# Kernel tuning notes

Hardware: AMD Instinct MI355X
Metric: run time of the kernel (lower is better)

## Reference

```python
import jax, jax.numpy as jnp
import numpy as np

EPSILON = 1e-8
MAX_WEIGHT = 0.15
N_ITER = 20
STEP_SIZE = 0.05
B, P = 32768, 45


def _simplex_projection(w):
    # clamp + renormalize, done twice (differentiable approximation)
    w = jnp.clip(w, 0.0, MAX_WEIGHT)
    w = w / (jnp.sum(w, axis=-1, keepdims=True) + EPSILON)
    w = jnp.clip(w, 0.0, MAX_WEIGHT)
    w = w / (jnp.sum(w, axis=-1, keepdims=True) + EPSILON)
    return w


def setup_inputs() -> dict:
    key = jax.random.key(0)
    k1, k2 = jax.random.split(key, 2)
    # SPD-ish covariance for a well-behaved iterative solve
    A = jax.random.normal(k1, (B, P, P), dtype=jnp.float32) * 0.1
    sigma = jnp.einsum('bij,bkj->bik', A, A) + 0.1 * jnp.eye(P, dtype=jnp.float32)
    beta = jax.nn.softmax(jax.random.normal(k2, (B, P), dtype=jnp.float32), axis=-1)
    w_prev = jnp.full((B, P), 1.0 / P, dtype=jnp.float32)
    return {
        'sigma': sigma,
        'beta': beta,
        'w_prev': w_prev,
        'log_lambda_sparse': jnp.asarray(-3.0, dtype=jnp.float32),
        'log_lambda_turnover': jnp.asarray(-2.0, dtype=jnp.float32),
    }


def reference(sigma, beta, w_prev, log_lambda_sparse, log_lambda_turnover):
    Bb, Pp = beta.shape
    lam_s = jnp.exp(log_lambda_sparse)
    lam_t = jnp.exp(log_lambda_turnover)
    w0 = jnp.full((Bb, Pp), 1.0 / Pp, dtype=sigma.dtype)

    def step(w, _):
        Sw = jnp.einsum('bij,bj->bi', sigma, w)  # [B,P]
        grad = 2.0 * Sw - beta + lam_s * jnp.sign(w) + 2.0 * lam_t * (w - w_prev)
        w = _simplex_projection(w - STEP_SIZE * grad)
        return w, None

    w, _ = jax.lax.scan(step, w0, None, length=N_ITER)
    return w
```

## Files before the change

kernel.cpp:

```cpp
#include <hip/hip_runtime.h>
#include <math.h>

#define P 45
#define N_ITER 20

template<int CTRL>
__device__ __forceinline__ float dpp_add(float x) {
    int xi = __builtin_bit_cast(int, x);
    int yi = __builtin_amdgcn_update_dpp(0, xi, CTRL, 0xF, 0xF, true);
    return x + __builtin_bit_cast(float, yi);
}

__device__ __forceinline__ float wave_sum_bcast(float x) {
    x = dpp_add<0x111>(x);
    x = dpp_add<0x112>(x);
    x = dpp_add<0x114>(x);
    x = dpp_add<0x118>(x);
    x = dpp_add<0x142>(x);
    x = dpp_add<0x143>(x);
    int si = __builtin_amdgcn_readlane(__builtin_bit_cast(int, x), 63);
    return __builtin_bit_cast(float, si);
}

__device__ __forceinline__ float clamp015(float x) {
    return __builtin_amdgcn_fmed3f(x, 0.0f, 0.15f);
}

__global__ __launch_bounds__(64, 6) void drb_kernel(
    const float* __restrict__ sigma,
    const float* __restrict__ beta,
    const float* __restrict__ w_prev,
    const float* __restrict__ lls,
    const float* __restrict__ llt,
    float* __restrict__ out)
{
    const int b    = blockIdx.x;
    const int lane = threadIdx.x;
    const bool active = lane < P;

    const float lam_s  = expf(lls[0]);
    const float lam_t2 = 2.0f * expf(llt[0]);

    float base = 0.0f;
    if (active) {
        const float bet = beta[(size_t)b * P + lane];
        const float wp  = w_prev[(size_t)b * P + lane];
        base = -bet - lam_t2 * wp;
    }

    {
    }
    const int cidx = active ? lane : (P - 1);
    const float* sp = sigma + (size_t)b * (P * P) + cidx;
    float row[P];
    #pragma unroll
    for (int j = 0; j < P; ++j) {
        float v = sp[(size_t)j * P];
        row[j] = active ? v : 0.0f;
    }
    #pragma unroll
    for (int j = 0; j < P; ++j) asm volatile("" : "+v"(row[j]));

    float c = active ? (float)(1.0 / 45.0) : 0.0f;

    for (int it = 0; it < N_ITER; ++it) {
        const int ci = __builtin_bit_cast(int, c);

        float cs[P];
        #pragma unroll
        for (int j = 0; j < P; ++j)
            cs[j] = __builtin_bit_cast(float, __builtin_amdgcn_readlane(ci, j));

        const float s2 = wave_sum_bcast(c);
        const float r  = __builtin_amdgcn_rcpf(s2 + 1e-8f);

        float acc0 = 0.0f, acc1 = 0.0f, acc2 = 0.0f;
        #pragma unroll
        for (int j = 0; j < P; j += 3) {
            acc0 = fmaf(row[j],     cs[j],     acc0);
            acc1 = fmaf(row[j + 1], cs[j + 1], acc1);
            acc2 = fmaf(row[j + 2], cs[j + 2], acc2);
        }
        const float acc = (acc0 + acc1) + acc2;

        const float t = c * r;
        float g = fmaf(lam_t2, t, base);
        g += (c > 0.0f) ? lam_s : 0.0f;
        g  = fmaf(r + r, acc, g);
        const float x = fmaf(-0.05f, g, t);

        const float a  = clamp015(x);
        const float s1 = wave_sum_bcast(a);
        const float r1 = __builtin_amdgcn_rcpf(s1 + 1e-8f);
        c = clamp015(a * r1);
    }

    const float sf = wave_sum_bcast(c);
    const float rf = __builtin_amdgcn_rcpf(sf + 1e-8f);
    if (active) out[(size_t)b * P + lane] = c * rf;
}

extern "C" void kernel_launch(void* const* d_in, const int* in_sizes, int n_in,
                              void* d_out, int out_size, void* d_ws, size_t ws_size,
                              hipStream_t stream) {
    const float* sigma  = (const float*)d_in[0];
    const float* beta   = (const float*)d_in[1];
    const float* w_prev = (const float*)d_in[2];
    const float* lls    = (const float*)d_in[3];
    const float* llt    = (const float*)d_in[4];
    float* out = (float*)d_out;

    const int B = in_sizes[1] / P;
    drb_kernel<<<B, 64, 0, stream>>>(sigma, beta, w_prev, lls, llt, out);
}
```

Before: 395.8 us.

## Broadcast weights via LDS with packed FMA and fold sum into matvec

Each iteration now broadcasts the weight vector through double-buffered shared memory instead of issuing 45 readlane instructions. Each lane holds its sigma row as packed float pairs and does the mat-vec with packed FMAs over 128-bit LDS reads. An extra lane holding all ones computes the vector sum inside the same mat-vec, which removes one wave reduction per iteration. It adds a barrier per iteration and LDS traffic, and drops the occupancy hint from the launch bounds.

```diff
diff --git a/kernel.cpp b/kernel.cpp
--- a/kernel.cpp
+++ b/kernel.cpp
@@ -3,6 +3,9 @@
 
 #define P 45
 #define N_ITER 20
+
+typedef float v2f __attribute__((ext_vector_type(2)));
+typedef float v4f __attribute__((ext_vector_type(4)));
 
 template<int CTRL>
 __device__ __forceinline__ float dpp_add(float x) {
@@ -26,7 +29,7 @@
     return __builtin_amdgcn_fmed3f(x, 0.0f, 0.15f);
 }
 
-__global__ __launch_bounds__(64, 6) void drb_kernel(
+__global__ __launch_bounds__(64) void drb_kernel(
     const float* __restrict__ sigma,
     const float* __restrict__ beta,
     const float* __restrict__ w_prev,
@@ -43,50 +46,68 @@
 
     float base = 0.0f;
     if (active) {
-        const float bet = beta[(size_t)b * P + lane];
-        const float wp  = w_prev[(size_t)b * P + lane];
-        base = -bet - lam_t2 * wp;
+        base = -beta[(size_t)b * P + lane]
+               - lam_t2 * w_prev[(size_t)b * P + lane];
     }
 
-    {
-    }
-    const int cidx = active ? lane : (P - 1);
+    const int cidx = active ? lane : 0;
     const float* sp = sigma + (size_t)b * (P * P) + cidx;
-    float row[P];
+    float rv[P + 1];
     #pragma unroll
     for (int j = 0; j < P; ++j) {
         float v = sp[(size_t)j * P];
-        row[j] = active ? v : 0.0f;
+        rv[j] = active ? v : 0.0f;
+    }
+    rv[P] = 0.0f;
+    const bool ones = (lane == P);
+    v2f row2[23];
+    #pragma unroll
+    for (int k = 0; k < 23; ++k) {
+        float lo = ones ? 1.0f : rv[2 * k];
+        float hi = (2 * k + 1 < P) ? (ones ? 1.0f : rv[2 * k + 1]) : 0.0f;
+        v2f t; t.x = lo; t.y = hi;
+        row2[k] = t;
     }
     #pragma unroll
-    for (int j = 0; j < P; ++j) asm volatile("" : "+v"(row[j]));
+    for (int k = 0; k < 23; ++k) asm volatile("" : "+v"(row2[k]));
+
+    __shared__ __align__(16) float sh[128];
 
     float c = active ? (float)(1.0 / 45.0) : 0.0f;
 
     for (int it = 0; it < N_ITER; ++it) {
-        const int ci = __builtin_bit_cast(int, c);
+        float* shb = sh + ((it & 1) << 6);
+        shb[lane] = c;
+        __syncthreads();
+        const v4f* shv = (const v4f*)shb;
 
-        float cs[P];
+        v2f acc0; acc0.x = 0.0f; acc0.y = 0.0f;
+        v2f acc1 = acc0, acc2 = acc0;
         #pragma unroll
-        for (int j = 0; j < P; ++j)
-            cs[j] = __builtin_bit_cast(float, __builtin_amdgcn_readlane(ci, j));
+        for (int k = 0; k < 11; ++k) {
+            v4f q = shv[k];
+            v2f lo; lo.x = q.x; lo.y = q.y;
+            v2f hi; hi.x = q.z; hi.y = q.w;
+            acc0 = __builtin_elementwise_fma(row2[2 * k],     lo, acc0);
+            acc1 = __builtin_elementwise_fma(row2[2 * k + 1], hi, acc1);
+        }
+        {
+            v4f q = shv[11];
+            v2f lo; lo.x = q.x; lo.y = q.y;
+            acc2 = __builtin_elementwise_fma(row2[22], lo, acc2);
+        }
+        v2f am = acc0 + acc1;
+        am = am + acc2;
+        const float acc = am.x + am.y;
 
-        const float s2 = wave_sum_bcast(c);
-        const float r  = __builtin_amdgcn_rcpf(s2 + 1e-8f);
-
-        float acc0 = 0.0f, acc1 = 0.0f, acc2 = 0.0f;
-        #pragma unroll
-        for (int j = 0; j < P; j += 3) {
-            acc0 = fmaf(row[j],     cs[j],     acc0);
-            acc1 = fmaf(row[j + 1], cs[j + 1], acc1);
-            acc2 = fmaf(row[j + 2], cs[j + 2], acc2);
-        }
-        const float acc = (acc0 + acc1) + acc2;
+        const float s2 = __builtin_bit_cast(float,
+            __builtin_amdgcn_readlane(__builtin_bit_cast(int, acc), P));
+        const float r = __builtin_amdgcn_rcpf(s2 + 1e-8f);
 
         const float t = c * r;
         float g = fmaf(lam_t2, t, base);
         g += (c > 0.0f) ? lam_s : 0.0f;
-        g  = fmaf(r + r, acc, g);
+        g = fmaf(r + r, acc, g);
         const float x = fmaf(-0.05f, g, t);
 
         const float a  = clamp015(x);
```

Result: faster. 377.2 us (-4.7%).
